# Kernel optimization log

Measured on AMD Instinct MI355X. Metric: run time of the kernel, lower is better.

Reference implementation:

```python
import jax, jax.numpy as jnp
import numpy as np
from jax import lax

K = 3  # AdaConv kernel_size inside conv_block


def conv2d(x, w, b, pad):
    # x: (B,C,H,W), w: (O,I,kh,kw) -> NCHW conv with symmetric padding
    y = lax.conv_general_dilated(x, w, (1, 1), [(pad, pad), (pad, pad)],
                                 dimension_numbers=('NCHW', 'OIHW', 'NCHW'))
    return y + b[None, :, None, None]


def unfold3(x):
    # nn.Unfold(kernel=3, pad=1): patches ordered channel-major then (kh,kw) row-major
    B, C, H, W = x.shape
    xp = jnp.pad(x, ((0, 0), (0, 0), (1, 1), (1, 1)))
    return jnp.stack([xp[:, :, i:i + H, j:j + W]
                      for i in range(K) for j in range(K)], axis=2)  # (B,C,9,H,W)


def adaconv(x, mask, aw_w, aw_b, mt_w, mt_b, c_w, c_b):
    # groups=1, groups_channels=out_ch in this configuration
    weight = conv2d(mask, aw_w, aw_b, pad=2)          # (B, 9, H, W)
    x = conv2d(x, c_w, c_b, pad=1)                    # (B, out_ch, H, W)
    p = unfold3(x)                                    # (B, out_ch, 9, H, W)
    out = jnp.einsum('bkhw,bckhw->bchw', weight, p)   # per-pixel adaptive conv
    mask2 = conv2d(mask, mt_w, mt_b, pad=2)
    return out, mask2


def lrelu(x):
    return jax.nn.leaky_relu(x, 0.01)


def setup_inputs() -> dict:
    key = jax.random.key(0)
    ks = jax.random.split(key, 20)
    B, Cin, Cout, Mi, Mo, H, W = 2, 64, 64, 64, 64, 256, 256
    s = 0.05
    d = {
        'x': jax.random.normal(ks[0], (B, Cin, H, W), jnp.float32),
        'mask': jax.random.normal(ks[1], (B, Mi, H, W), jnp.float32),
        # AdaConv 1 (in_ch->out_ch, mask_in->mask_out)
        'aw1_w': jax.random.normal(ks[2], (K * K, Mi, 2 * K - 1, 2 * K - 1), jnp.float32) * s,
        'aw1_b': jax.random.normal(ks[3], (K * K,), jnp.float32) * s,
        'mt1_w': jax.random.normal(ks[4], (Mo, Mi, 2 * K - 1, 2 * K - 1), jnp.float32) * s,
        'mt1_b': jax.random.normal(ks[5], (Mo,), jnp.float32) * s,
        'c1_w': jax.random.normal(ks[6], (Cout, Cin, K, K), jnp.float32) * s,
        'c1_b': jax.random.normal(ks[7], (Cout,), jnp.float32) * s,
        # AdaConv 2 (out_ch->out_ch, mask_out->mask_out)
        'aw2_w': jax.random.normal(ks[8], (K * K, Mo, 2 * K - 1, 2 * K - 1), jnp.float32) * s,
        'aw2_b': jax.random.normal(ks[9], (K * K,), jnp.float32) * s,
        'mt2_w': jax.random.normal(ks[10], (Mo, Mo, 2 * K - 1, 2 * K - 1), jnp.float32) * s,
        'mt2_b': jax.random.normal(ks[11], (Mo,), jnp.float32) * s,
        'c2_w': jax.random.normal(ks[12], (Cout, Cout, K, K), jnp.float32) * s,
        'c2_b': jax.random.normal(ks[13], (Cout,), jnp.float32) * s,
        # 1x1 residual conv
        'cr_w': jax.random.normal(ks[14], (Cout, Cin, 1, 1), jnp.float32) * s,
        'cr_b': jax.random.normal(ks[15], (Cout,), jnp.float32) * s,
    }
    return d


def reference(x, mask, aw1_w, aw1_b, mt1_w, mt1_b, c1_w, c1_b,
              aw2_w, aw2_b, mt2_w, mt2_b, c2_w, c2_b, cr_w, cr_b):
    res = conv2d(x, cr_w, cr_b, pad=0)
    x, mask = adaconv(x, mask, aw1_w, aw1_b, mt1_w, mt1_b, c1_w, c1_b)
    x, mask = lrelu(x), lrelu(mask)
    x, mask = adaconv(x, mask, aw2_w, aw2_b, mt2_w, mt2_b, c2_w, c2_b)
    x, mask = lrelu(x), lrelu(mask)
    return (x + res, mask)
```

## Files before the change

### kernel.cpp

```cpp
#include <hip/hip_runtime.h>

#define HWSZ 65536
#define CCH  64

typedef __bf16 bf16x8 __attribute__((ext_vector_type(8)));
typedef __bf16 bf16x4 __attribute__((ext_vector_type(4)));
typedef float  f32x4  __attribute__((ext_vector_type(4)));

__device__ inline void gload_lds16(const void* g, void* l) {
    __builtin_amdgcn_global_load_lds(
        (const __attribute__((address_space(1))) void*)g,
        (__attribute__((address_space(3))) void*)l, 16, 0, 0);
}


__device__ void cvt_body(int cb, const float* __restrict__ src,
                         __bf16* __restrict__ dst)
{
    int p  = cb * 256 + threadIdx.x;
    int b  = p >> 16, hw = p & 65535;
    const float* sp = src + (((size_t)b * 64) << 16) + hw;
    __bf16* dp = dst + (size_t)p * 64;
    #pragma unroll
    for (int c8 = 0; c8 < 8; ++c8) {
        bf16x8 v8;
        #pragma unroll
        for (int j = 0; j < 8; ++j)
            v8[j] = (__bf16)sp[(size_t)(c8 * 8 + j) << 16];
        *(bf16x8*)(dp + c8 * 8) = v8;
    }
}

__device__ void prep3_body(int cb, const float* __restrict__ src,
                           __bf16* __restrict__ dst)
{
    int t = cb * 256 + threadIdx.x;
    if (t >= 2 * 9 * 2048) return;
    int j  = t & 7;
    int u  = (t >> 3) & 255;
    int q  = t >> 11;
    int s  = q % 9, ci = q / 9;
    int dx = s / 3, dy = s % 3;
    int k  = dy * 3 + dx;
    int r  = u >> 3;
    int v  = (u & 7) ^ (r & 7);
    int o  = 2 * r + (v >> 2);
    int g  = v & 3;
    int i  = ci * 32 + g * 8 + j;
    dst[t] = (__bf16)src[((size_t)o * 64 + i) * 9 + k];
}

__device__ void prep1_body(int cb, const float* __restrict__ src,
                           __bf16* __restrict__ dst)
{
    int t = cb * 256 + threadIdx.x;
    if (t >= 2 * 2048) return;
    int j  = t & 7;
    int u  = (t >> 3) & 255;
    int ci = t >> 11;
    int r  = u >> 3;
    int v  = (u & 7) ^ (r & 7);
    int o  = 2 * r + (v >> 2);
    int g  = v & 3;
    int i  = ci * 32 + g * 8 + j;
    dst[t] = (__bf16)src[(size_t)o * 64 + i];
}

__device__ void prepF_body(int cb, const float* __restrict__ mt,
                           const float* __restrict__ aw, __bf16* __restrict__ dst)
{
    int t = cb * 256 + threadIdx.x;
    if (t >= 2 * 25 * 3072) return;
    int j  = t & 7;
    int u  = (t >> 3) % 384;
    int q  = t / 3072;
    int s  = q % 25, ci = q / 25;
    int dx = s / 5, dy = s % 5;
    int k  = dy * 5 + dx;
    int r  = u >> 3;
    int v  = (u & 7) ^ (r & 7);
    int o  = 2 * r + (v >> 2);
    int g  = v & 3;
    int i  = ci * 32 + g * 8 + j;
    float val = 0.f;
    if (o < 64)      val = mt[((size_t)o * 64 + i) * 25 + k];
    else if (o < 73) val = aw[((size_t)(o - 64) * 64 + i) * 25 + k];
    dst[t] = (__bf16)val;
}

__global__ __launch_bounds__(256) void k_prep(
    const float* x, const float* mask,
    const float* c1w, const float* c2w,
    const float* mt1w, const float* aw1w,
    const float* mt2w, const float* aw2w,
    const float* crw,
    __bf16* xh, __bf16* mh,
    __bf16* wbc1, __bf16* wbc2, __bf16* wbF1, __bf16* wbF2, __bf16* wbcr)
{
    int bid = blockIdx.x;
    if      (bid < 512)  cvt_body(bid, x, xh);
    else if (bid < 1024) cvt_body(bid - 512, mask, mh);
    else if (bid < 1168) prep3_body(bid - 1024, c1w, wbc1);
    else if (bid < 1312) prep3_body(bid - 1168, c2w, wbc2);
    else if (bid < 1912) prepF_body(bid - 1312, mt1w, aw1w, wbF1);
    else if (bid < 2512) prepF_body(bid - 1912, mt2w, aw2w, wbF2);
    else                 prep1_body(bid - 2512, crw, wbcr);
}

template<int EPI>
__global__ __launch_bounds__(256) void k_conv5(
    const __bf16* __restrict__ xh, const __bf16* __restrict__ wb,
    const float* __restrict__ bias, const float* __restrict__ bias2,
    float* __restrict__ outf, __bf16* __restrict__ outh,
    float* __restrict__ out2)
{
    constexpr int TW    = 20;
    constexpr int NPIX  = 400;
    constexpr int NPIX2 = NPIX / 2;
    constexpr int MFT   = 5;
    constexpr int SLICE = 6144;

    __shared__ __align__(16) __bf16 lx[NPIX2 * 64];
    __shared__ __align__(16) __bf16 lw[5 * 3072];
    __shared__ float lb[80];

    const int t    = threadIdx.x;
    const int w0   = blockIdx.x * 16, h0 = blockIdx.y * 16, b = blockIdx.z;
    const int wvv  = t >> 6;
    const int lane = t & 63;
    const int px   = lane & 15;
    const int g    = lane >> 4;

    auto STAGE_GRP = [&](int ci, int grp) {
        const char* gs = (const char*)wb + (size_t)(ci * 25 + grp * 5) * SLICE;
        #pragma unroll
        for (int r = 0; r < 8; ++r) {
            int u = r * 256 + wvv * 64;
            if (u < 1920)
                gload_lds16(gs + (u + lane) * 16, (char*)lw + u * 16);
        }
    };

    f32x4 acc[MFT][4];
    #pragma unroll
    for (int m = 0; m < MFT; ++m)
        #pragma unroll
        for (int nf = 0; nf < 4; ++nf)
            acc[m][nf] = (f32x4){0.f, 0.f, 0.f, 0.f};

    bf16x8 zv;
    #pragma unroll
    for (int j = 0; j < 8; ++j) zv[j] = (__bf16)0.f;

    for (int ci = 0; ci < 2; ++ci) {
        STAGE_GRP(ci, 0);
        if (ci == 0) {
            if (t < 64) lb[t] = bias[t];
            if (t >= 64 && t < 80) lb[t] = (t - 64 < 9) ? bias2[t - 64] : 0.f;
        }

        #pragma unroll
        for (int xi = 0; xi < 7; ++xi) {
            int e = xi * 256 + t;
            if (e < NPIX * 4) {
                int pix = e >> 2, c4 = e & 3;
                int sy = pix / TW, sx = pix - sy * TW;
                int gy = h0 + sy - 2, gx = w0 + sx - 2;
                bool ok = (unsigned)gy < 256u && (unsigned)gx < 256u;
                bf16x8 v8 = zv;
                if (ok) v8 = *(const bf16x8*)(xh + ((((size_t)b << 16) + gy * 256 + gx) << 6)
                                              + ci * 32 + c4 * 8);
                int row = pix >> 1;
                int off = row * 128 + (((((pix & 1) << 2) + c4) ^ (row & 7)) << 4);
                *(bf16x8*)((char*)lx + off) = v8;
            }
        }
        __syncthreads();

        #pragma unroll
        for (int dxg = 0; dxg < 5; ++dxg) {
            bf16x8 bfr[9];
            #pragma unroll
            for (int r = 0; r < 9; ++r) {
                int pix = (wvv * 4 + r) * TW + (px + dxg);
                int row = pix >> 1;
                int off = row * 128 + (((((pix & 1) << 2) + g) ^ (row & 7)) << 4);
                bfr[r] = *(const bf16x8*)((const char*)lx + off);
            }
            bf16x8 afr[5][MFT];
            #pragma unroll
            for (int dy = 0; dy < 5; ++dy)
                #pragma unroll
                for (int m = 0; m < MFT; ++m) {
                    int o = m * 16 + px;
                    int row = o >> 1;
                    int off = dy * SLICE + row * 128
                            + (((((o & 1) << 2) + g) ^ (row & 7)) << 4);
                    afr[dy][m] = *(const bf16x8*)((const char*)lw + off);
                }

            asm volatile("s_waitcnt lgkmcnt(0)" ::: "memory");
            __builtin_amdgcn_sched_barrier(0);
            __builtin_amdgcn_s_barrier();

            if (dxg < 4) STAGE_GRP(ci, dxg + 1);

            __builtin_amdgcn_s_setprio(1);
            #pragma unroll
            for (int dy = 0; dy < 5; ++dy)
                #pragma unroll
                for (int m = 0; m < MFT; ++m)
                    #pragma unroll
                    for (int nf = 0; nf < 4; ++nf)
                        acc[m][nf] = __builtin_amdgcn_mfma_f32_16x16x32_bf16(
                            afr[dy][m], bfr[nf + dy], acc[m][nf], 0, 0, 0);
            __builtin_amdgcn_s_setprio(0);

            asm volatile("s_waitcnt vmcnt(0)" ::: "memory");
            __builtin_amdgcn_sched_barrier(0);
            __builtin_amdgcn_s_barrier();
        }
    }

    #pragma unroll
    for (int m = 0; m < MFT; ++m) {
        #pragma unroll
        for (int nf = 0; nf < 4; ++nf) {
            int row = h0 + wvv * 4 + nf, col = w0 + px;
            if (m < 4) {
                float vj[4];
                #pragma unroll
                for (int j = 0; j < 4; ++j) {
                    float v = acc[m][nf][j] + lb[m * 16 + g * 4 + j];
                    vj[j] = v > 0.f ? v : 0.01f * v;
                }
                if constexpr (EPI == 0) {
                    bf16x4 pk;
                    #pragma unroll
                    for (int j = 0; j < 4; ++j) pk[j] = (__bf16)vj[j];
                    *(bf16x4*)(outh + ((((size_t)b << 16) + row * 256 + col) << 6)
                                    + m * 16 + g * 4) = pk;
                } else {
                    #pragma unroll
                    for (int j = 0; j < 4; ++j)
                        outf[((size_t)(b * 64 + m * 16 + g * 4 + j) << 16)
                             + row * 256 + col] = vj[j];
                }
            } else {
                #pragma unroll
                for (int j = 0; j < 4; ++j) {
                    int o2 = g * 4 + j;
                    if (o2 < 9)
                        out2[((size_t)(b * 9 + o2) << 16) + row * 256 + col]
                            = acc[m][nf][j] + lb[64 + o2];
                }
            }
        }
    }
}

__global__ __launch_bounds__(256) void k_conv3(
    const __bf16* __restrict__ xh, const __bf16* __restrict__ wb,
    const float* __restrict__ bias, __bf16* __restrict__ outh)
{
    constexpr int TW    = 18;
    constexpr int NPIX  = 324;
    constexpr int NPIX2 = 162;

    __shared__ __align__(16) __bf16 lx[NPIX2 * 64];
    __shared__ __align__(16) __bf16 lw[9 * 2048];
    __shared__ float lb[64];

    const int t    = threadIdx.x;
    const int w0   = blockIdx.x * 16, h0 = blockIdx.y * 16, b = blockIdx.z;
    const int wvv  = t >> 6;
    const int lane = t & 63;
    const int px   = lane & 15;
    const int g    = lane >> 4;

    f32x4 acc[4][4];
    #pragma unroll
    for (int m = 0; m < 4; ++m)
        #pragma unroll
        for (int nf = 0; nf < 4; ++nf)
            acc[m][nf] = (f32x4){0.f, 0.f, 0.f, 0.f};

    bf16x8 zv;
    #pragma unroll
    for (int j = 0; j < 8; ++j) zv[j] = (__bf16)0.f;

    for (int ci = 0; ci < 2; ++ci) {
        if (ci) __syncthreads();
        {
            const char* gs = (const char*)wb + (size_t)ci * 9 * 4096;
            #pragma unroll
            for (int r = 0; r < 9; ++r) {
                int ub = r * 256 + wvv * 64;
                gload_lds16(gs + (ub + lane) * 16, (char*)lw + ub * 16);
            }
        }
        if (ci == 0 && t < 64) lb[t] = bias[t];

        #pragma unroll
        for (int xi = 0; xi < 6; ++xi) {
            int e = xi * 256 + t;
            if (e < NPIX * 4) {
                int pix = e >> 2, c4 = e & 3;
                int sy = pix / TW, sx = pix - sy * TW;
                int gy = h0 + sy - 1, gx = w0 + sx - 1;
                bool ok = (unsigned)gy < 256u && (unsigned)gx < 256u;
                bf16x8 v8 = zv;
                if (ok) v8 = *(const bf16x8*)(xh + ((((size_t)b << 16) + gy * 256 + gx) << 6)
                                              + ci * 32 + c4 * 8);
                int row = pix >> 1;
                int off = row * 128 + (((((pix & 1) << 2) + c4) ^ (row & 7)) << 4);
                *(bf16x8*)((char*)lx + off) = v8;
            }
        }
        __syncthreads();

        #pragma unroll
        for (int dxg = 0; dxg < 3; ++dxg) {
            bf16x8 bfr[6];
            #pragma unroll
            for (int r = 0; r < 6; ++r) {
                int pix = (wvv * 4 + r) * TW + (px + dxg);
                int row = pix >> 1;
                int off = row * 128 + (((((pix & 1) << 2) + g) ^ (row & 7)) << 4);
                bfr[r] = *(const bf16x8*)((const char*)lx + off);
            }
            #pragma unroll
            for (int dy = 0; dy < 3; ++dy) {
                const __bf16* lwb = lw + (dxg * 3 + dy) * 2048;
                bf16x8 afr[4];
                #pragma unroll
                for (int m = 0; m < 4; ++m) {
                    int o = m * 16 + px;
                    int row = o >> 1;
                    int off = row * 128 + (((((o & 1) << 2) + g) ^ (row & 7)) << 4);
                    afr[m] = *(const bf16x8*)((const char*)lwb + off);
                }
                __builtin_amdgcn_s_setprio(1);
                #pragma unroll
                for (int m = 0; m < 4; ++m)
                    #pragma unroll
                    for (int nf = 0; nf < 4; ++nf)
                        acc[m][nf] = __builtin_amdgcn_mfma_f32_16x16x32_bf16(
                            afr[m], bfr[nf + dy], acc[m][nf], 0, 0, 0);
                __builtin_amdgcn_s_setprio(0);
            }
        }
    }

    #pragma unroll
    for (int m = 0; m < 4; ++m) {
        #pragma unroll
        for (int nf = 0; nf < 4; ++nf) {
            int row = h0 + wvv * 4 + nf, col = w0 + px;
            bf16x4 pk;
            #pragma unroll
            for (int j = 0; j < 4; ++j) {
                float v = acc[m][nf][j] + lb[m * 16 + g * 4 + j];
                pk[j] = (__bf16)v;
            }
            *(bf16x4*)(outh + ((((size_t)b << 16) + row * 256 + col) << 6)
                            + m * 16 + g * 4) = pk;
        }
    }
}

__global__ __launch_bounds__(256) void k_conv1(
    const __bf16* __restrict__ xh, const __bf16* __restrict__ wb,
    const float* __restrict__ bias, __bf16* __restrict__ outh)
{
    constexpr int NPIX2 = 128;

    __shared__ __align__(16) __bf16 lx[NPIX2 * 64];
    __shared__ __align__(16) __bf16 lw[2048];
    __shared__ float lb[64];

    const int t    = threadIdx.x;
    const int w0   = blockIdx.x * 16, h0 = blockIdx.y * 16, b = blockIdx.z;
    const int wvv  = t >> 6;
    const int lane = t & 63;
    const int px   = lane & 15;
    const int g    = lane >> 4;

    f32x4 acc[4][4];
    #pragma unroll
    for (int m = 0; m < 4; ++m)
        #pragma unroll
        for (int nf = 0; nf < 4; ++nf)
            acc[m][nf] = (f32x4){0.f, 0.f, 0.f, 0.f};

    for (int ci = 0; ci < 2; ++ci) {
        if (ci) __syncthreads();
        {
            const char* gs = (const char*)wb + (size_t)ci * 4096;
            int ub = wvv * 64;
            gload_lds16(gs + (ub + lane) * 16, (char*)lw + ub * 16);
        }
        if (ci == 0 && t < 64) lb[t] = bias[t];

        #pragma unroll
        for (int xi = 0; xi < 4; ++xi) {
            int e = xi * 256 + t;
            int pix = e >> 2, c4 = e & 3;
            int gy = h0 + (pix >> 4), gx = w0 + (pix & 15);
            bf16x8 v8 = *(const bf16x8*)(xh + ((((size_t)b << 16) + gy * 256 + gx) << 6)
                                         + ci * 32 + c4 * 8);
            int row = pix >> 1;
            int off = row * 128 + (((((pix & 1) << 2) + c4) ^ (row & 7)) << 4);
            *(bf16x8*)((char*)lx + off) = v8;
        }
        __syncthreads();

        bf16x8 bfr[4];
        #pragma unroll
        for (int nf = 0; nf < 4; ++nf) {
            int pix = (wvv * 4 + nf) * 16 + px;
            int row = pix >> 1;
            int off = row * 128 + (((((pix & 1) << 2) + g) ^ (row & 7)) << 4);
            bfr[nf] = *(const bf16x8*)((const char*)lx + off);
        }
        bf16x8 afr[4];
        #pragma unroll
        for (int m = 0; m < 4; ++m) {
            int o = m * 16 + px;
            int row = o >> 1;
            int off = row * 128 + (((((o & 1) << 2) + g) ^ (row & 7)) << 4);
            afr[m] = *(const bf16x8*)((const char*)lw + off);
        }
        #pragma unroll
        for (int m = 0; m < 4; ++m)
            #pragma unroll
            for (int nf = 0; nf < 4; ++nf)
                acc[m][nf] = __builtin_amdgcn_mfma_f32_16x16x32_bf16(
                    afr[m], bfr[nf], acc[m][nf], 0, 0, 0);
    }

    #pragma unroll
    for (int m = 0; m < 4; ++m) {
        #pragma unroll
        for (int nf = 0; nf < 4; ++nf) {
            int row = h0 + wvv * 4 + nf, col = w0 + px;
            bf16x4 pk;
            #pragma unroll
            for (int j = 0; j < 4; ++j)
                pk[j] = (__bf16)(acc[m][nf][j] + lb[m * 16 + g * 4 + j]);
            *(bf16x4*)(outh + ((((size_t)b << 16) + row * 256 + col) << 6)
                            + m * 16 + g * 4) = pk;
        }
    }
}

__global__ __launch_bounds__(256, 4) void k_ada1(
    const float* __restrict__ wgt, const __bf16* __restrict__ xin,
    __bf16* __restrict__ outh)
{
    int t  = threadIdx.x;
    int pg = t >> 3, c8 = t & 7;
    int p  = blockIdx.x * 32 + pg;
    int b  = p >> 16, hw = p & 65535;
    int h  = hw >> 8, wc = hw & 255;

    const float* wp = wgt + ((size_t)(b * 9) << 16) + hw;
    const __bf16* cen = xin + (size_t)p * 64 + c8 * 8;

    float wk[9];
    const __bf16* nbp[9];
    #pragma unroll
    for (int dy = 0; dy < 3; ++dy)
        #pragma unroll
        for (int dx = 0; dx < 3; ++dx) {
            int k = dy * 3 + dx;
            bool ok = ((unsigned)(h + dy - 1) < 256u) &&
                      ((unsigned)(wc + dx - 1) < 256u);
            wk[k]  = ok ? wp[(size_t)k << 16] : 0.f;
            nbp[k] = ok ? cen + ((dy - 1) * 256 + (dx - 1)) * 64 : cen;
        }

    float acc[8] = {0.f,0.f,0.f,0.f,0.f,0.f,0.f,0.f};
    #pragma unroll
    for (int k = 0; k < 9; ++k) {
        bf16x8 v8 = *(const bf16x8*)nbp[k];
        float w = wk[k];
        #pragma unroll
        for (int j = 0; j < 8; ++j) acc[j] += w * (float)v8[j];
    }

    bf16x8 o8;
    #pragma unroll
    for (int j = 0; j < 8; ++j) {
        float v = acc[j];
        o8[j] = (__bf16)(v > 0.f ? v : 0.01f * v);
    }
    *(bf16x8*)(outh + (size_t)p * 64 + c8 * 8) = o8;
}

__global__ __launch_bounds__(256, 4) void k_ada2(
    const float* __restrict__ wgt, const __bf16* __restrict__ x2h,
    const __bf16* __restrict__ resh, float* __restrict__ outf)
{
    __shared__ float ls[32 * 65];

    int t  = threadIdx.x;
    int pg = t >> 3, c8 = t & 7;
    int p  = blockIdx.x * 32 + pg;
    int b  = p >> 16, hw = p & 65535;
    int h  = hw >> 8, wc = hw & 255;

    const float* wp = wgt + ((size_t)(b * 9) << 16) + hw;
    const __bf16* cen = x2h + (size_t)p * 64 + c8 * 8;

    float wk[9];
    const __bf16* nbp[9];
    #pragma unroll
    for (int dy = 0; dy < 3; ++dy)
        #pragma unroll
        for (int dx = 0; dx < 3; ++dx) {
            int k = dy * 3 + dx;
            bool ok = ((unsigned)(h + dy - 1) < 256u) &&
                      ((unsigned)(wc + dx - 1) < 256u);
            wk[k]  = ok ? wp[(size_t)k << 16] : 0.f;
            nbp[k] = ok ? cen + ((dy - 1) * 256 + (dx - 1)) * 64 : cen;
        }

    float acc[8] = {0.f,0.f,0.f,0.f,0.f,0.f,0.f,0.f};
    #pragma unroll
    for (int k = 0; k < 9; ++k) {
        bf16x8 v8 = *(const bf16x8*)nbp[k];
        float w = wk[k];
        #pragma unroll
        for (int j = 0; j < 8; ++j) acc[j] += w * (float)v8[j];
    }

    bf16x8 r8 = *(const bf16x8*)(resh + (size_t)p * 64 + c8 * 8);
    #pragma unroll
    for (int j = 0; j < 8; ++j) {
        float v = acc[j];
        v = v > 0.f ? v : 0.01f * v;
        ls[pg * 65 + c8 * 8 + j] = v + (float)r8[j];
    }
    __syncthreads();

    int pbase = blockIdx.x * 32;
    int bb    = pbase >> 16, hwb = pbase & 65535;
    int pix   = t & 31, cq = t >> 5;
    #pragma unroll
    for (int i = 0; i < 8; ++i) {
        int c = i * 8 + cq;
        size_t oi = ((size_t)(bb * 64 + c) << 16) + hwb + pix;
        outf[oi] = ls[pix * 65 + c];
    }
}

extern "C" void kernel_launch(void* const* d_in, const int* in_sizes, int n_in,
                              void* d_out, int out_size, void* d_ws, size_t ws_size,
                              hipStream_t stream)
{
    const float* x     = (const float*)d_in[0];
    const float* mask  = (const float*)d_in[1];
    const float* aw1_w = (const float*)d_in[2];
    const float* aw1_b = (const float*)d_in[3];
    const float* mt1_w = (const float*)d_in[4];
    const float* mt1_b = (const float*)d_in[5];
    const float* c1_w  = (const float*)d_in[6];
    const float* c1_b  = (const float*)d_in[7];
    const float* aw2_w = (const float*)d_in[8];
    const float* aw2_b = (const float*)d_in[9];
    const float* mt2_w = (const float*)d_in[10];
    const float* mt2_b = (const float*)d_in[11];
    const float* c2_w  = (const float*)d_in[12];
    const float* c2_b  = (const float*)d_in[13];
    const float* cr_w  = (const float*)d_in[14];
    const float* cr_b  = (const float*)d_in[15];

    float* out_x = (float*)d_out;
    float* out_m = (float*)d_out + 8388608;

    float*  wgt   = (float*)d_ws;
    __bf16* xh    = (__bf16*)((char*)d_ws + 4718592);
    __bf16* mh    = (__bf16*)((char*)d_ws + 21495808);
    __bf16* x2h   = mh;
    __bf16* wbase = (__bf16*)((char*)d_ws + 38273024);
    __bf16* wb_c1 = wbase;
    __bf16* wb_c2 = wbase + 36864;
    __bf16* wb_F1 = wbase + 73728;
    __bf16* wb_F2 = wbase + 227328;
    __bf16* wb_cr = wbase + 380928;
    __bf16* resh  = (__bf16*)((char*)d_ws + 39043072);

    __bf16* maska_h = (__bf16*)out_x;
    __bf16* xa_h    = (__bf16*)out_x + 8388608;
    __bf16* x1_h    = (__bf16*)out_m;

    dim3 blk(256);
    dim3 gconv(16, 16, 2);
    dim3 gada(4096);

    k_prep<<<dim3(2528), blk, 0, stream>>>(x, mask, c1_w, c2_w,
        mt1_w, aw1_w, mt2_w, aw2_w, cr_w,
        xh, mh, wb_c1, wb_c2, wb_F1, wb_F2, wb_cr);

    k_conv5<0><<<gconv, blk, 0, stream>>>(mh, wb_F1, mt1_b, aw1_b,
                                          nullptr, maska_h, wgt);
    k_conv3<<<gconv, blk, 0, stream>>>(xh, wb_c1, c1_b, x1_h);
    k_ada1<<<gada, blk, 0, stream>>>(wgt, x1_h, xa_h);
    k_conv5<1><<<gconv, blk, 0, stream>>>(maska_h, wb_F2, mt2_b, aw2_b,
                                          out_m, nullptr, wgt);
    k_conv3<<<gconv, blk, 0, stream>>>(xa_h, wb_c2, c2_b, x2h);
    k_conv1<<<gconv, blk, 0, stream>>>(xh, wb_cr, cr_b, resh);
    k_ada2<<<gada, blk, 0, stream>>>(wgt, x2h, resh, out_x);
}
```

Before: 178.5 us.

## Shrink conv5 tile to 16x8 and double-buffer per-tap weight slices

The 5x5 conv kernel now processes 16x8 output tiles, launching twice as many blocks, with each wave covering 2 rows instead of 4. Weights are staged one tap at a time into a two-slot LDS ring buffer, prefetched two taps ahead with partial vmcnt waits, instead of five-tap groups. This shrinks LDS use and registers for better occupancy and finer-grained overlap. In exchange, each block reloads more halo per output and runs 25 barrier-separated steps with fewer MFMAs between barriers.

```diff
diff --git a/kernel.cpp b/kernel.cpp
--- a/kernel.cpp
+++ b/kernel.cpp
@@ -115,37 +115,40 @@
     float* __restrict__ out2)
 {
     constexpr int TW    = 20;
-    constexpr int NPIX  = 400;
+    constexpr int TH    = 12;
+    constexpr int NPIX  = TW * TH;
     constexpr int NPIX2 = NPIX / 2;
+    constexpr int KK    = 25;
+    constexpr int SLICE = 6144;
     constexpr int MFT   = 5;
-    constexpr int SLICE = 6144;
 
     __shared__ __align__(16) __bf16 lx[NPIX2 * 64];
-    __shared__ __align__(16) __bf16 lw[5 * 3072];
+    __shared__ __align__(16) __bf16 lw[2][96 * 32];
     __shared__ float lb[80];
 
     const int t    = threadIdx.x;
-    const int w0   = blockIdx.x * 16, h0 = blockIdx.y * 16, b = blockIdx.z;
+    const int w0   = blockIdx.x * 16, h0 = blockIdx.y * 8, b = blockIdx.z;
     const int wvv  = t >> 6;
     const int lane = t & 63;
     const int px   = lane & 15;
     const int g    = lane >> 4;
 
-    auto STAGE_GRP = [&](int ci, int grp) {
-        const char* gs = (const char*)wb + (size_t)(ci * 25 + grp * 5) * SLICE;
-        #pragma unroll
-        for (int r = 0; r < 8; ++r) {
-            int u = r * 256 + wvv * 64;
-            if (u < 1920)
-                gload_lds16(gs + (u + lane) * 16, (char*)lw + u * 16);
+    auto STAGE = [&](int ci, int s, int buf) {
+        const char* gs = (const char*)wb + (size_t)(ci * KK + s) * SLICE;
+        if (wvv < 3) {
+            #pragma unroll
+            for (int r = 0; r < 2; ++r) {
+                int ub = wvv * 128 + r * 64;
+                gload_lds16(gs + (ub + lane) * 16, (char*)lw[buf] + ub * 16);
+            }
         }
     };
 
-    f32x4 acc[MFT][4];
+    f32x4 acc[MFT][2];
     #pragma unroll
     for (int m = 0; m < MFT; ++m)
         #pragma unroll
-        for (int nf = 0; nf < 4; ++nf)
+        for (int nf = 0; nf < 2; ++nf)
             acc[m][nf] = (f32x4){0.f, 0.f, 0.f, 0.f};
 
     bf16x8 zv;
@@ -153,14 +156,16 @@
     for (int j = 0; j < 8; ++j) zv[j] = (__bf16)0.f;
 
     for (int ci = 0; ci < 2; ++ci) {
-        STAGE_GRP(ci, 0);
+        if (ci) __syncthreads();
+        STAGE(ci, 0, 0);
+        STAGE(ci, 1, 1);
         if (ci == 0) {
             if (t < 64) lb[t] = bias[t];
             if (t >= 64 && t < 80) lb[t] = (t - 64 < 9) ? bias2[t - 64] : 0.f;
         }
 
         #pragma unroll
-        for (int xi = 0; xi < 7; ++xi) {
+        for (int xi = 0; xi < 4; ++xi) {
             int e = xi * 256 + t;
             if (e < NPIX * 4) {
                 int pix = e >> 2, c4 = e & 3;
@@ -178,45 +183,44 @@
         __syncthreads();
 
         #pragma unroll
-        for (int dxg = 0; dxg < 5; ++dxg) {
-            bf16x8 bfr[9];
-            #pragma unroll
-            for (int r = 0; r < 9; ++r) {
-                int pix = (wvv * 4 + r) * TW + (px + dxg);
+        for (int s = 0; s < KK; ++s) {
+            const __bf16* lwb = (s & 1) ? lw[1] : lw[0];
+            const int dx = s / 5, dy = s % 5;
+
+            bf16x8 bfr[2];
+            #pragma unroll
+            for (int nf = 0; nf < 2; ++nf) {
+                int pix = (wvv * 2 + nf + dy) * TW + (px + dx);
                 int row = pix >> 1;
                 int off = row * 128 + (((((pix & 1) << 2) + g) ^ (row & 7)) << 4);
-                bfr[r] = *(const bf16x8*)((const char*)lx + off);
-            }
-            bf16x8 afr[5][MFT];
-            #pragma unroll
-            for (int dy = 0; dy < 5; ++dy)
+                bfr[nf] = *(const bf16x8*)((const char*)lx + off);
+            }
+            bf16x8 afr[MFT];
+            #pragma unroll
+            for (int m = 0; m < MFT; ++m) {
+                int o = m * 16 + px;
+                int row = o >> 1;
+                int off = row * 128 + (((((o & 1) << 2) + g) ^ (row & 7)) << 4);
+                afr[m] = *(const bf16x8*)((const char*)lwb + off);
+            }
+            __builtin_amdgcn_s_setprio(1);
+            #pragma unroll
+            for (int m = 0; m < MFT; ++m)
                 #pragma unroll
-                for (int m = 0; m < MFT; ++m) {
-                    int o = m * 16 + px;
-                    int row = o >> 1;
-                    int off = dy * SLICE + row * 128
-                            + (((((o & 1) << 2) + g) ^ (row & 7)) << 4);
-                    afr[dy][m] = *(const bf16x8*)((const char*)lw + off);
-                }
+                for (int nf = 0; nf < 2; ++nf)
+                    acc[m][nf] = __builtin_amdgcn_mfma_f32_16x16x32_bf16(
+                        afr[m], bfr[nf], acc[m][nf], 0, 0, 0);
+            __builtin_amdgcn_s_setprio(0);
+
+            if (s == KK - 1) break;
 
             asm volatile("s_waitcnt lgkmcnt(0)" ::: "memory");
             __builtin_amdgcn_sched_barrier(0);
             __builtin_amdgcn_s_barrier();
-
-            if (dxg < 4) STAGE_GRP(ci, dxg + 1);
-
-            __builtin_amdgcn_s_setprio(1);
-            #pragma unroll
-            for (int dy = 0; dy < 5; ++dy)
-                #pragma unroll
-                for (int m = 0; m < MFT; ++m)
-                    #pragma unroll
-                    for (int nf = 0; nf < 4; ++nf)
-                        acc[m][nf] = __builtin_amdgcn_mfma_f32_16x16x32_bf16(
-                            afr[dy][m], bfr[nf + dy], acc[m][nf], 0, 0, 0);
-            __builtin_amdgcn_s_setprio(0);
-
-            asm volatile("s_waitcnt vmcnt(0)" ::: "memory");
+            bool issued = (s + 2 < KK);
+            if (issued) STAGE(ci, s + 2, s & 1);
+            if (issued && wvv < 3) asm volatile("s_waitcnt vmcnt(2)" ::: "memory");
+            else                   asm volatile("s_waitcnt vmcnt(0)" ::: "memory");
             __builtin_amdgcn_sched_barrier(0);
             __builtin_amdgcn_s_barrier();
         }
@@ -225,8 +229,8 @@
     #pragma unroll
     for (int m = 0; m < MFT; ++m) {
         #pragma unroll
-        for (int nf = 0; nf < 4; ++nf) {
-            int row = h0 + wvv * 4 + nf, col = w0 + px;
+        for (int nf = 0; nf < 2; ++nf) {
+            int row = h0 + wvv * 2 + nf, col = w0 + px;
             if (m < 4) {
                 float vj[4];
                 #pragma unroll
@@ -596,6 +600,7 @@
     __bf16* x1_h    = (__bf16*)out_m;
 
     dim3 blk(256);
+    dim3 gconv5(16, 32, 2);
     dim3 gconv(16, 16, 2);
     dim3 gada(4096);
 
@@ -603,12 +608,12 @@
         mt1_w, aw1_w, mt2_w, aw2_w, cr_w,
         xh, mh, wb_c1, wb_c2, wb_F1, wb_F2, wb_cr);
 
-    k_conv5<0><<<gconv, blk, 0, stream>>>(mh, wb_F1, mt1_b, aw1_b,
-                                          nullptr, maska_h, wgt);
+    k_conv5<0><<<gconv5, blk, 0, stream>>>(mh, wb_F1, mt1_b, aw1_b,
+                                           nullptr, maska_h, wgt);
     k_conv3<<<gconv, blk, 0, stream>>>(xh, wb_c1, c1_b, x1_h);
     k_ada1<<<gada, blk, 0, stream>>>(wgt, x1_h, xa_h);
-    k_conv5<1><<<gconv, blk, 0, stream>>>(maska_h, wb_F2, mt2_b, aw2_b,
-                                          out_m, nullptr, wgt);
+    k_conv5<1><<<gconv5, blk, 0, stream>>>(maska_h, wb_F2, mt2_b, aw2_b,
+                                           out_m, nullptr, wgt);
     k_conv3<<<gconv, blk, 0, stream>>>(xa_h, wb_c2, c2_b, x2h);
     k_conv1<<<gconv, blk, 0, stream>>>(xh, wb_cr, cr_b, resh);
     k_ada2<<<gada, blk, 0, stream>>>(wgt, x2h, resh, out_x);
```

After: 186.3 us. 4.3% more time.
